# Kernel optimization log

Hardware: AMD Instinct MI355X
Metric: run time of the kernel (lower is better)

The kernel has to match this reference:

```python
import jax, jax.numpy as jnp
import numpy as np

H = 32          # total heads
K = 8           # active heads per token
D = 128         # head_dim = embed_dim // active_heads
E = 1024        # embed_dim
S = 1024        # seq_len
MAX_SEQ = 8192
BASE = 10000.0
SCALE = D ** -0.5
LB_W = 0.01
ENT_W = 0.01


def _rope(v, cos, sin):
    # v: (T, D); cos/sin: (T, D)
    v1, v2 = v[:, : D // 2], v[:, D // 2:]
    rot = jnp.concatenate([-v2, v1], axis=-1)
    return v * cos + rot * sin


def setup_inputs() -> dict:
    key = jax.random.key(0)
    ks = jax.random.split(key, 6)
    x = jax.random.normal(ks[0], (1, S, E), jnp.float32)
    Wq = jax.random.normal(ks[1], (E, H * D), jnp.float32) * 0.02
    Wk = jax.random.normal(ks[2], (E, H * D), jnp.float32) * 0.02
    Wv = jax.random.normal(ks[3], (E, H * D), jnp.float32) * 0.02
    Wr = jax.random.normal(ks[4], (E, H), jnp.float32) * 0.02
    Wo = jax.random.normal(ks[5], (K * D, E), jnp.float32) * 0.02
    head_counts = jnp.zeros((1, H), jnp.int32)
    return {"x": x, "Wq": Wq, "Wk": Wk, "Wv": Wv, "Wr": Wr, "Wo": Wo,
            "head_counts": head_counts}


def reference(x, Wq, Wk, Wv, Wr, Wo, head_counts):
    # ---- routing (eval mode: no gumbel noise) ----
    logits = x @ Wr                                   # (1, S, H)
    soft_probs = jax.nn.softmax(logits, axis=-1)
    top_logits, head_idx = jax.lax.top_k(logits, K)   # (1, S, K)
    head_w = jax.nn.softmax(top_logits, axis=-1)      # (1, S, K)

    # ---- aux loss ----
    primary = head_idx[..., 0]                        # (1, S)
    one_hot_p = jax.nn.one_hot(primary, H, dtype=jnp.float32)
    f = one_hot_p.mean(axis=1)                        # (1, H)
    p = soft_probs.mean(axis=1)                       # (1, H)
    balance = H * (f * p).sum(axis=-1).mean()
    entropy = -(soft_probs * jnp.log(soft_probs + 1e-8)).sum(axis=-1)
    entropy_loss = -entropy.mean()
    z_loss = (jax.nn.logsumexp(logits, axis=-1) ** 2).mean() * 0.01
    aux_loss = LB_W * balance + ENT_W * entropy_loss + z_loss

    # ---- projections + per-token gather of selected heads ----
    q_all = (x @ Wq).reshape(1, S, H, D)
    k_all = (x @ Wk).reshape(1, S, H, D)
    v_all = (x @ Wv).reshape(1, S, H, D)
    gidx = head_idx[..., None]                        # (1, S, K, 1)
    q = jnp.take_along_axis(q_all, gidx, axis=2)[0].reshape(S * K, D)
    k = jnp.take_along_axis(k_all, gidx, axis=2)[0].reshape(S * K, D)
    v = jnp.take_along_axis(v_all, gidx, axis=2)[0].reshape(S * K, D)

    heads_flat = head_idx[0].reshape(S * K)           # (T,)

    # rank of each dispatched token within its head (exclusive prefix count)
    oh = jax.nn.one_hot(heads_flat, H, dtype=jnp.int32)   # (T, H)
    excl = jnp.cumsum(oh, axis=0) - oh
    rank = jnp.take_along_axis(excl, heads_flat[:, None], axis=1)[:, 0]
    positions = rank + head_counts[0, heads_flat]
    positions = jnp.clip(positions, 0, MAX_SEQ - 1)

    # ---- per-head RoPE with per-head position counters ----
    inv_freq = 1.0 / (BASE ** (jnp.arange(0, D, 2, dtype=jnp.float32) / D))
    freqs = positions.astype(jnp.float32)[:, None] * inv_freq[None, :]
    emb = jnp.concatenate([freqs, freqs], axis=-1)    # (T, D)
    cos, sin = jnp.cos(emb), jnp.sin(emb)
    q = _rope(q, cos, sin)
    k = _rope(k, cos, sin)

    # ---- block-diagonal-causal attention (same head, earlier dispatch order) ----
    idx = jnp.arange(S * K)
    mask = (heads_flat[:, None] == heads_flat[None, :]) & (idx[None, :] <= idx[:, None])
    scores = (q @ k.T) * SCALE                        # (T, T)
    scores = jnp.where(mask, scores, jnp.float32(-1e30))
    attn = jax.nn.softmax(scores, axis=-1)
    out = attn @ v                                    # (T, D)

    # ---- combine with routing weights + output projection ----
    out = out.reshape(S, K, D) * head_w[0][..., None]
    out = out.reshape(S, K * D) @ Wo                  # (S, E)
    output = out[None]                                # (1, S, E)

    updated_counts = head_counts + oh.sum(axis=0)[None]
    return output, updated_counts, aux_loss
```

## Files before the change

kernel.cpp:

```cpp
#include <hip/hip_runtime.h>
#include <math.h>

#define S 1024
#define E 1024
#define H 32
#define KSEL 8
#define D 128
#define HD 4096
#define SK 8192
#define MAXL 1024
#define CAP 9216
#define ATTN_SCALE 0.08838834764831845f
#define SSTR 36
#define PSTR 40

typedef _Float16 half8 __attribute__((ext_vector_type(8)));
typedef _Float16 half4 __attribute__((ext_vector_type(4)));
typedef float floatx4 __attribute__((ext_vector_type(4)));
typedef float floatx16 __attribute__((ext_vector_type(16)));
typedef float f4 __attribute__((ext_vector_type(4)));

#define GLOAD_LDS16(gsrc, ldst) \
    __builtin_amdgcn_global_load_lds( \
        (const __attribute__((address_space(1))) void*)(gsrc), \
        (__attribute__((address_space(3))) void*)(ldst), 16, 0, 0)

__global__ __launch_bounds__(256) void router_kernel(
    const float* __restrict__ x, const float* __restrict__ Wr,
    int* __restrict__ head_idx, float* __restrict__ head_w,
    float* __restrict__ pbuf, float* __restrict__ entz,
    _Float16* __restrict__ xh)
{
    int tid = threadIdx.x;
    int s = blockIdx.x * 4 + (tid >> 6);
    int lane = tid & 63;
    int h = lane & 31, half = lane >> 5;
    const float* xr = x + (size_t)s * E + half * 512;
    const float* wr = Wr + (size_t)(half * 512) * H + h;
    float a0 = 0.f, a1 = 0.f, a2 = 0.f, a3 = 0.f;
    #pragma unroll 4
    for (int e = 0; e < 512; e += 4) {
        a0 += xr[e]     * wr[e * H];
        a1 += xr[e + 1] * wr[(e + 1) * H];
        a2 += xr[e + 2] * wr[(e + 2) * H];
        a3 += xr[e + 3] * wr[(e + 3) * H];
    }
    float acc = (a0 + a1) + (a2 + a3);
    acc += __shfl_xor(acc, 32, 64);
    float logit = acc;
    float m = logit;
    #pragma unroll
    for (int off = 16; off; off >>= 1) m = fmaxf(m, __shfl_xor(m, off, 64));
    float ex = expf(logit - m);
    float Z = ex;
    #pragma unroll
    for (int off = 16; off; off >>= 1) Z += __shfl_xor(Z, off, 64);
    float p = ex / Z;
    float es = p * logf(p + 1e-8f);
    #pragma unroll
    for (int off = 16; off; off >>= 1) es += __shfl_xor(es, off, 64);
    float lse = m + logf(Z);
    float lv = logit;
    float tv[KSEL]; int ti[KSEL];
    #pragma unroll
    for (int j = 0; j < KSEL; ++j) {
        float bv = lv; int bi = h;
        #pragma unroll
        for (int off = 16; off; off >>= 1) {
            float ov = __shfl_xor(bv, off, 64);
            int oi = __shfl_xor(bi, off, 64);
            if (ov > bv || (ov == bv && oi < bi)) { bv = ov; bi = oi; }
        }
        tv[j] = bv; ti[j] = bi;
        if (h == bi) lv = -INFINITY;
    }
    float Z2 = 0.f;
    #pragma unroll
    for (int j = 0; j < KSEL; ++j) Z2 += expf(tv[j] - tv[0]);
    if (lane < 32) pbuf[s * 32 + lane] = p;
    if (lane == 0) {
        entz[s * 2]     = es;
        entz[s * 2 + 1] = lse * lse;
        #pragma unroll
        for (int j = 0; j < KSEL; ++j) {
            head_idx[s * KSEL + j] = ti[j];
            head_w[s * KSEL + j]   = expf(tv[j] - tv[0]) / Z2;
        }
    }
    const float* xrow = x + (size_t)s * E;
    _Float16* xhrow = xh + (size_t)s * E;
    #pragma unroll
    for (int t = 0; t < 4; ++t) {
        int e = t * 256 + lane * 4;
        f4 v = *(const f4*)&xrow[e];
        half4 o;
        o.x = (_Float16)v.x; o.y = (_Float16)v.y; o.z = (_Float16)v.z; o.w = (_Float16)v.w;
        *(half4*)&xhrow[e] = o;
    }
}

__global__ __launch_bounds__(256) void order_conv_kernel(
    const int* __restrict__ head_idx, const int* __restrict__ head_counts,
    int* __restrict__ order, int* __restrict__ hlen, float* __restrict__ out_counts,
    const float* __restrict__ pbuf, const float* __restrict__ entz,
    float* __restrict__ out_aux,
    const float* __restrict__ Wq, const float* __restrict__ Wk,
    const float* __restrict__ Wv, const float* __restrict__ Wo,
    _Float16* __restrict__ Wqkt, _Float16* __restrict__ Wot)
{
    int bid = blockIdx.x, tid = threadIdx.x;
    if (bid >= 33) {
        int cb = bid - 33;
        int z = cb >> 10, rem = cb & 1023;
        if (z == 3 && (rem >> 4) >= 16) return;
        const float* W = (z == 0) ? Wq : (z == 1) ? Wk : (z == 2) ? Wv : Wo;
        _Float16* T = (z < 3) ? (Wqkt + (size_t)z * HD * E) : Wot;
        int C = (z < 3) ? HD : 1024;
        int r0 = (rem & 15) * 64, c0 = (rem >> 4) * 64;
        __shared__ float tile[64][65];
        #pragma unroll
        for (int p = 0; p < 4; ++p) {
            int idx = p * 256 + tid;
            int r = idx >> 4, cq = (idx & 15) * 4;
            f4 v = *(const f4*)&W[(size_t)(r0 + r) * C + c0 + cq];
            tile[r][cq] = v.x; tile[r][cq + 1] = v.y; tile[r][cq + 2] = v.z; tile[r][cq + 3] = v.w;
        }
        __syncthreads();
        #pragma unroll
        for (int p = 0; p < 2; ++p) {
            int idx = p * 256 + tid;
            int c = idx >> 3, r8 = (idx & 7) * 8;
            half8 o;
            #pragma unroll
            for (int j = 0; j < 8; ++j) o[j] = (_Float16)tile[r8 + j][c];
            *(half8*)&T[(size_t)(c0 + c) * 1024 + r0 + r8] = o;
        }
        return;
    }
    if (bid == H) {
        int hh = tid & 31, grp = tid >> 5;
        __shared__ float red[256], red2[256];
        __shared__ float psum[32];
        __shared__ int hist[32];
        if (tid < 32) hist[tid] = 0;
        float ps = 0.f;
        for (int s = grp; s < S; s += 8) ps += pbuf[s * 32 + hh];
        red[tid] = ps;
        float es = 0.f, zs = 0.f;
        for (int s = tid; s < S; s += 256) { es += entz[s * 2]; zs += entz[s * 2 + 1]; }
        red2[tid] = es;
        __syncthreads();
        if (grp == 0) {
            float v = 0.f;
            #pragma unroll
            for (int j = 0; j < 8; ++j) v += red[j * 32 + hh];
            psum[hh] = v;
        }
        __syncthreads();
        red[tid] = zs;
        for (int s = tid; s < S; s += 256)
            atomicAdd(&hist[head_idx[s * KSEL]], 1);
        __syncthreads();
        for (int stp = 128; stp; stp >>= 1) {
            if (tid < stp) { red[tid] += red[tid + stp]; red2[tid] += red2[tid + stp]; }
            __syncthreads();
        }
        if (tid == 0) {
            float bal = 0.f;
            for (int j = 0; j < H; ++j)
                bal += ((float)hist[j] / (float)S) * (psum[j] / (float)S);
            bal *= (float)H;
            float ent_loss = red2[0] / (float)S;
            float z = red[0] / (float)S * 0.01f;
            out_aux[0] = 0.01f * bal + 0.01f * ent_loss + z;
        }
        return;
    }
    int h = bid;
    int wave = tid >> 6, lane = tid & 63;
    __shared__ int wtot[4];
    int base = 0;
    int hc = head_counts[h];
    int v = head_idx[tid];
    for (int c0 = 0; c0 < SK; c0 += 256) {
        int vn = (c0 + 256 < SK) ? head_idx[c0 + 256 + tid] : 0;
        bool pred = (v == h);
        unsigned long long mask = __ballot(pred);
        int within = __popcll(mask & ((1ull << lane) - 1ull));
        if (lane == 0) wtot[wave] = __popcll(mask);
        __syncthreads();
        int pre = 0, tot = 0;
        #pragma unroll
        for (int w = 0; w < 4; ++w) { int t = wtot[w]; if (w < wave) pre += t; tot += t; }
        if (pred) order[h * MAXL + base + pre + within] = c0 + tid;
        base += tot;
        __syncthreads();
        v = vn;
    }
    if (tid == 0) {
        hlen[h] = base;
        out_counts[h] = (float)(hc + base);
    }
}

__global__ __launch_bounds__(256) void qkv_mfma(
    const _Float16* __restrict__ xh, const _Float16* __restrict__ Wt,
    const int* __restrict__ order, const int* __restrict__ hlen,
    const int* __restrict__ head_counts,
    _Float16* __restrict__ qh, _Float16* __restrict__ kh, _Float16* __restrict__ vT)
{
    int xid = blockIdx.x;
    int qkv = xid >> 5, h = xid & 31;
    int rt = blockIdx.y;
    int len = hlen[h];
    int row0 = rt * 64;
    if (row0 >= len) return;
    int hb = 0;
    for (int i = 0; i < h; ++i) hb += (hlen[i] + 31) & ~31;
    int lenp = (len + 31) & ~31;
    int tid = threadIdx.x, wave = tid >> 6, lane = tid & 63;
    int wm = wave >> 1, wn = wave & 1;
    int l32 = lane & 31, g = lane >> 5;

    __shared__ _Float16 Bs[2][128 * 64];

    int arow_g = row0 + wm * 32 + l32;
    int tok = (arow_g < len) ? (order[h * MAXL + arow_g] >> 3) : 0;
    const _Float16* aptr = xh + (size_t)tok * E;

    const _Float16* Wb = Wt + (size_t)((qkv * H + h) * D) * E;

    auto stageB = [&](int buf, int k0) {
        #pragma unroll
        for (int it = 0; it < 4; ++it) {
            int f = it * 256 + tid;
            int row = f >> 3, c = f & 7;
            int sc = c ^ (row & 7);
            const _Float16* src = Wb + (size_t)row * E + k0 + sc * 8;
            GLOAD_LDS16(src, &Bs[buf][f * 8]);
        }
    };

    floatx16 acc[2] = {};
    half8 a_cur[4], a_nxt[4];
    #pragma unroll
    for (int ks = 0; ks < 4; ++ks)
        a_cur[ks] = *(const half8*)(aptr + ks * 16 + g * 8);

    auto compute = [&](int buf, half8* a) {
        #pragma unroll
        for (int ks = 0; ks < 4; ++ks) {
            int wchunk = ks * 2 + g;
            #pragma unroll
            for (int nf = 0; nf < 2; ++nf) {
                int brow = wn * 64 + nf * 32 + l32;
                half8 bf = *(const half8*)&Bs[buf][brow * 64 + (wchunk ^ (brow & 7)) * 8];
                acc[nf] = __builtin_amdgcn_mfma_f32_32x32x16_f16(a[ks], bf, acc[nf], 0, 0, 0);
            }
        }
    };

    stageB(0, 0);
    __syncthreads();
    int buf = 0;
    for (int k0 = 64; k0 < E; k0 += 64) {
        stageB(buf ^ 1, k0);
        #pragma unroll
        for (int ks = 0; ks < 4; ++ks)
            a_nxt[ks] = *(const half8*)(aptr + k0 + ks * 16 + g * 8);
        compute(buf, a_cur);
        __syncthreads();
        buf ^= 1;
        #pragma unroll
        for (int ks = 0; ks < 4; ++ks) a_cur[ks] = a_nxt[ks];
    }
    compute(buf, a_cur);

    if (qkv < 2) {
        _Float16* dst = (qkv == 0) ? qh : kh;
        float* scr = (float*)&Bs[0][0];
        __syncthreads();
        #pragma unroll
        for (int nf = 0; nf < 2; ++nf) {
            int col = wn * 64 + nf * 32 + l32;
            #pragma unroll
            for (int reg = 0; reg < 16; ++reg) {
                int rl = wm * 32 + (reg & 3) + 8 * (reg >> 2) + 4 * g;
                scr[rl * 128 + col] = acc[nf][reg];
            }
        }
        __syncthreads();
        int hc = head_counts[h];
        #pragma unroll
        for (int pass = 0; pass < 16; ++pass) {
            int idx = pass * 256 + tid;
            int r = idx >> 6, d2 = idx & 63;
            int slot = row0 + r;
            if (slot < len) {
                float v1 = scr[r * 128 + d2], v2 = scr[r * 128 + 64 + d2];
                int p = slot + hc;
                p = p < 0 ? 0 : (p > 8191 ? 8191 : p);
                float inv = exp2f((float)d2 * -0.20762050f);
                float ang = (float)p * inv;
                float cs = cosf(ang), sn = sinf(ang);
                _Float16* dp = dst + ((size_t)hb + slot) * D;
                dp[d2]      = (_Float16)(v1 * cs - v2 * sn);
                dp[d2 + 64] = (_Float16)(v2 * cs + v1 * sn);
            }
        }
    } else {
        #pragma unroll
        for (int nf = 0; nf < 2; ++nf) {
            int col = wn * 64 + nf * 32 + l32;
            #pragma unroll
            for (int q4 = 0; q4 < 4; ++q4) {
                int slot0 = row0 + wm * 32 + 8 * q4 + 4 * g;
                _Float16* vp = vT + (size_t)hb * D + (size_t)col * lenp + slot0;
                if (slot0 + 3 < len) {
                    half4 o;
                    o.x = (_Float16)acc[nf][q4 * 4 + 0];
                    o.y = (_Float16)acc[nf][q4 * 4 + 1];
                    o.z = (_Float16)acc[nf][q4 * 4 + 2];
                    o.w = (_Float16)acc[nf][q4 * 4 + 3];
                    *(half4*)vp = o;
                } else {
                    #pragma unroll
                    for (int r2 = 0; r2 < 4; ++r2)
                        if (slot0 + r2 < len) vp[r2] = (_Float16)acc[nf][q4 * 4 + r2];
                }
            }
        }
    }
}

__global__ __launch_bounds__(128) void attn_mfma(
    const _Float16* __restrict__ qh, const _Float16* __restrict__ kh,
    const _Float16* __restrict__ vT,
    const int* __restrict__ order, const int* __restrict__ hlen,
    const float* __restrict__ head_w, _Float16* __restrict__ ao)
{
    int h = blockIdx.x >> 5, qt = blockIdx.x & 31;
    int len = hlen[h];
    int row0 = qt * 32;
    if (row0 >= len) return;
    int hb = 0;
    for (int i = 0; i < h; ++i) hb += (hlen[i] + 31) & ~31;
    int lenp = (len + 31) & ~31;
    int tid = threadIdx.x;
    int w = tid >> 6, lane = tid & 63;
    int l32 = lane & 31, g = lane >> 5;
    int srow = lane >> 1, shalf = lane & 1;

    __shared__ float Sld[2][32 * SSTR];
    __shared__ _Float16 Pld[2][32 * PSTR];
    __shared__ float alphaLd[2][32];
    __shared__ float mlLd[32][4];
    __shared__ float facLd[32][3];
    __shared__ int flatLd[32];
    __shared__ float Obuf[32][128];

    if (tid < 32) {
        int r = row0 + tid;
        flatLd[tid] = (r < len) ? order[h * MAXL + r] : -1;
    }

    const _Float16* qrow = qh + ((size_t)hb + row0 + l32) * D;
    half8 qf[8];
    #pragma unroll
    for (int t = 0; t < 8; ++t) qf[t] = *(const half8*)(qrow + t * 16 + g * 8);

    floatx16 O[4] = {};
    float m_run = -INFINITY, l_run = 0.f;

    if (w <= qt) {
        half8 kf[8], kfn[8], vv[8];
        {
            const _Float16* krow = kh + ((size_t)hb + w * 32 + l32) * D;
            #pragma unroll
            for (int t = 0; t < 8; ++t) kf[t] = *(const half8*)(krow + t * 16 + g * 8);
        }
        for (int kt = w; kt <= qt; kt += 2) {
            int col0 = kt * 32;
            floatx16 Sc = {};
            #pragma unroll
            for (int t = 0; t < 8; ++t)
                Sc = __builtin_amdgcn_mfma_f32_32x32x16_f16(qf[t], kf[t], Sc, 0, 0, 0);
            #pragma unroll
            for (int nt = 0; nt < 4; ++nt) {
                const _Float16* vp = vT + (size_t)hb * D + (size_t)(nt * 32 + l32) * lenp + col0;
                vv[nt * 2]     = *(const half8*)(vp + g * 8);
                vv[nt * 2 + 1] = *(const half8*)(vp + 16 + g * 8);
            }
            if (kt + 2 <= qt) {
                const _Float16* krow = kh + ((size_t)hb + col0 + 64 + l32) * D;
                #pragma unroll
                for (int t = 0; t < 8; ++t) kfn[t] = *(const half8*)(krow + t * 16 + g * 8);
            }
            bool diag = (kt == qt);
            #pragma unroll
            for (int reg = 0; reg < 16; ++reg) {
                int row = (reg & 3) + 8 * (reg >> 2) + 4 * g;
                float s = Sc[reg] * ATTN_SCALE;
                if (diag && l32 > row) s = -1e30f;
                Sld[w][row * SSTR + l32] = s;
            }
            __builtin_amdgcn_wave_barrier();
            const float* sp = &Sld[w][srow * SSTR + shalf * 16];
            float va[16];
            *(f4*)(va)      = *(const f4*)(sp);
            *(f4*)(va + 4)  = *(const f4*)(sp + 4);
            *(f4*)(va + 8)  = *(const f4*)(sp + 8);
            *(f4*)(va + 12) = *(const f4*)(sp + 12);
            float mt_ = va[0];
            #pragma unroll
            for (int j = 1; j < 16; ++j) mt_ = fmaxf(mt_, va[j]);
            mt_ = fmaxf(mt_, __shfl_xor(mt_, 1, 64));
            float m_new = fmaxf(m_run, mt_);
            float alpha = __expf(m_run - m_new);
            float p[16], tsum = 0.f;
            #pragma unroll
            for (int j = 0; j < 16; ++j) { p[j] = __expf(va[j] - m_new); tsum += p[j]; }
            tsum += __shfl_xor(tsum, 1, 64);
            l_run = l_run * alpha + tsum;
            m_run = m_new;
            half8 ph0, ph1;
            #pragma unroll
            for (int j = 0; j < 8; ++j) { ph0[j] = (_Float16)p[j]; ph1[j] = (_Float16)p[j + 8]; }
            *(half8*)&Pld[w][srow * PSTR + shalf * 16]     = ph0;
            *(half8*)&Pld[w][srow * PSTR + shalf * 16 + 8] = ph1;
            if (shalf == 0) alphaLd[w][srow] = alpha;
            __builtin_amdgcn_wave_barrier();
            f4 al[4];
            #pragma unroll
            for (int qq = 0; qq < 4; ++qq) al[qq] = *(const f4*)&alphaLd[w][4 * g + 8 * qq];
            #pragma unroll
            for (int reg = 0; reg < 16; ++reg) {
                float av = al[reg >> 2][reg & 3];
                O[0][reg] *= av; O[1][reg] *= av; O[2][reg] *= av; O[3][reg] *= av;
            }
            half8 pf0 = *(const half8*)&Pld[w][l32 * PSTR + g * 8];
            half8 pf1 = *(const half8*)&Pld[w][l32 * PSTR + 16 + g * 8];
            #pragma unroll
            for (int nt = 0; nt < 4; ++nt) {
                O[nt] = __builtin_amdgcn_mfma_f32_32x32x16_f16(pf0, vv[nt * 2],     O[nt], 0, 0, 0);
                O[nt] = __builtin_amdgcn_mfma_f32_32x32x16_f16(pf1, vv[nt * 2 + 1], O[nt], 0, 0, 0);
            }
            __builtin_amdgcn_wave_barrier();
            #pragma unroll
            for (int t = 0; t < 8; ++t) kf[t] = kfn[t];
        }
    }
    if (shalf == 0) { mlLd[srow][w * 2] = m_run; mlLd[srow][w * 2 + 1] = l_run; }
    __syncthreads();
    if (tid < 32) {
        float m0 = mlLd[tid][0], l0 = mlLd[tid][1];
        float m1 = mlLd[tid][2], l1 = mlLd[tid][3];
        float ms = fmaxf(m0, m1);
        float f0 = __expf(m0 - ms), f1 = __expf(m1 - ms);
        float lt = f0 * l0 + f1 * l1;
        int flat = flatLd[tid];
        float hw = (flat >= 0) ? head_w[flat] : 0.f;
        facLd[tid][0] = f1;
        facLd[tid][1] = hw / lt;
        facLd[tid][2] = f0;
    }
    __syncthreads();
    if (w == 1) {
        #pragma unroll
        for (int nt = 0; nt < 4; ++nt) {
            int col = nt * 32 + l32;
            #pragma unroll
            for (int reg = 0; reg < 16; ++reg) {
                int row = (reg & 3) + 8 * (reg >> 2) + 4 * g;
                Obuf[row][col] = O[nt][reg] * facLd[row][0];
            }
        }
    }
    __syncthreads();
    if (w == 0) {
        #pragma unroll
        for (int nt = 0; nt < 4; ++nt) {
            int col = nt * 32 + l32;
            #pragma unroll
            for (int reg = 0; reg < 16; ++reg) {
                int row = (reg & 3) + 8 * (reg >> 2) + 4 * g;
                int flat = flatLd[row];
                if (flat >= 0) {
                    float val = (O[nt][reg] * facLd[row][2] + Obuf[row][col]) * facLd[row][1];
                    ao[(size_t)flat * D + col] = (_Float16)val;
                }
            }
        }
    }
}

__global__ __launch_bounds__(256) void out_mfma(
    const _Float16* __restrict__ A, const _Float16* __restrict__ Bt,
    float* __restrict__ C)
{
    int n0 = blockIdx.x * 64, m0 = blockIdx.y * 64;
    int tid = threadIdx.x, wave = tid >> 6, lane = tid & 63;
    int wm = wave >> 1, wn = wave & 1;
    int l32 = lane & 31, g = lane >> 5;

    __shared__ _Float16 Bs[2][64 * 64];

    const _Float16* aptr = A + (size_t)(m0 + wm * 32 + l32) * 1024;

    auto stageB = [&](int buf, int k0) {
        #pragma unroll
        for (int it = 0; it < 2; ++it) {
            int f = it * 256 + tid;
            int row = f >> 3, c = f & 7;
            int sc = c ^ (row & 7);
            GLOAD_LDS16(Bt + (size_t)(n0 + row) * 1024 + k0 + sc * 8, &Bs[buf][f * 8]);
        }
    };

    floatx16 acc = {};
    int brow = wn * 32 + l32;
    half8 a_cur[4], a_nxt[4];
    #pragma unroll
    for (int ks = 0; ks < 4; ++ks)
        a_cur[ks] = *(const half8*)(aptr + ks * 16 + g * 8);

    auto compute = [&](int buf, half8* a) {
        #pragma unroll
        for (int ks = 0; ks < 4; ++ks) {
            int wchunk = ks * 2 + g;
            half8 bf = *(const half8*)&Bs[buf][brow * 64 + (wchunk ^ (brow & 7)) * 8];
            acc = __builtin_amdgcn_mfma_f32_32x32x16_f16(a[ks], bf, acc, 0, 0, 0);
        }
    };

    stageB(0, 0);
    __syncthreads();
    int buf = 0;
    for (int k0 = 64; k0 < 1024; k0 += 64) {
        stageB(buf ^ 1, k0);
        #pragma unroll
        for (int ks = 0; ks < 4; ++ks)
            a_nxt[ks] = *(const half8*)(aptr + k0 + ks * 16 + g * 8);
        compute(buf, a_cur);
        __syncthreads();
        buf ^= 1;
        #pragma unroll
        for (int ks = 0; ks < 4; ++ks) a_cur[ks] = a_nxt[ks];
    }
    compute(buf, a_cur);

    int col = n0 + wn * 32 + l32;
    #pragma unroll
    for (int reg = 0; reg < 16; ++reg) {
        int row = m0 + wm * 32 + (reg & 3) + 8 * (reg >> 2) + 4 * g;
        C[(size_t)row * 1024 + col] = acc[reg];
    }
}

extern "C" void kernel_launch(void* const* d_in, const int* in_sizes, int n_in,
                              void* d_out, int out_size, void* d_ws, size_t ws_size,
                              hipStream_t stream)
{
    const float* x  = (const float*)d_in[0];
    const float* Wq = (const float*)d_in[1];
    const float* Wk = (const float*)d_in[2];
    const float* Wv = (const float*)d_in[3];
    const float* Wr = (const float*)d_in[4];
    const float* Wo = (const float*)d_in[5];
    const int* head_counts = (const int*)d_in[6];
    float* out = (float*)d_out;

    float* head_w = (float*)d_ws;
    float* pbuf   = head_w + SK;
    float* entz   = pbuf + S * 32;
    int* head_idx = (int*)(entz + S * 2);
    int* order    = head_idx + SK;
    int* hlen     = order + H * MAXL;
    _Float16* xh   = (_Float16*)(hlen + 64);
    _Float16* aoh  = xh + (size_t)S * E;
    _Float16* Wqkt = aoh + (size_t)SK * D;
    _Float16* Wot  = Wqkt + (size_t)3 * HD * E;
    _Float16* qh   = Wot + (size_t)1024 * 1024;
    _Float16* kh   = qh + (size_t)CAP * D;
    _Float16* vT   = kh + (size_t)CAP * D;

    router_kernel<<<S / 4, 256, 0, stream>>>(x, Wr, head_idx, head_w, pbuf, entz, xh);
    order_conv_kernel<<<33 + 4096, 256, 0, stream>>>(head_idx, head_counts, order, hlen,
                                                     out + (size_t)S * E, pbuf, entz,
                                                     out + (size_t)S * E + H,
                                                     Wq, Wk, Wv, Wo, Wqkt, Wot);
    qkv_mfma<<<dim3(96, 16), 256, 0, stream>>>(xh, Wqkt, order, hlen, head_counts,
                                               qh, kh, vT);
    attn_mfma<<<H * 32, 128, 0, stream>>>(qh, kh, vT, order, hlen, head_w, aoh);
    out_mfma<<<dim3(16, 16), 256, 0, stream>>>(aoh, Wot, out);
}
```

Measured before the change: 220.1 us.

## Move weight conversion into router kernel and batch per-head scan chunks

The fp32-to-fp16 weight transpose/convert work moves out of the order kernel and into the router kernel as extra blocks. It now uses 128x128 fp16 tiles with an XOR-swizzled LDS layout instead of 64x64 fp32 tiles, so conversion overlaps routing and the scan kernel no longer waits behind 4000+ conversion blocks. The per-head order scan handles four 256-element chunks per iteration, cutting the number of barrier round trips by four. The risk is larger LDS use per conversion block (32KB) and fewer, heavier blocks.

```diff
diff --git a/kernel.cpp b/kernel.cpp
--- a/kernel.cpp
+++ b/kernel.cpp
@@ -14,6 +14,9 @@
 #define SSTR 36
 #define PSTR 40
 
+#define NROUTER 256
+#define NCONV 832
+
 typedef _Float16 half8 __attribute__((ext_vector_type(8)));
 typedef _Float16 half4 __attribute__((ext_vector_type(4)));
 typedef float floatx4 __attribute__((ext_vector_type(4)));
@@ -25,14 +28,54 @@
         (const __attribute__((address_space(1))) void*)(gsrc), \
         (__attribute__((address_space(3))) void*)(ldst), 16, 0, 0)
 
-__global__ __launch_bounds__(256) void router_kernel(
+__global__ __launch_bounds__(256) void router_conv_kernel(
     const float* __restrict__ x, const float* __restrict__ Wr,
     int* __restrict__ head_idx, float* __restrict__ head_w,
     float* __restrict__ pbuf, float* __restrict__ entz,
-    _Float16* __restrict__ xh)
+    _Float16* __restrict__ xh,
+    const float* __restrict__ Wq, const float* __restrict__ Wk,
+    const float* __restrict__ Wv, const float* __restrict__ Wo,
+    _Float16* __restrict__ Wqkt, _Float16* __restrict__ Wot)
 {
-    int tid = threadIdx.x;
-    int s = blockIdx.x * 4 + (tid >> 6);
+    int bid = blockIdx.x, tid = threadIdx.x;
+    if (bid >= NROUTER) {
+        __shared__ _Float16 tl[128 * 128];
+        int cb = bid - NROUTER;
+        int z, rem;
+        if (cb < 768) { z = cb >> 8; rem = cb & 255; }
+        else          { z = 3;       rem = cb - 768; }
+        const float* W = (z == 0) ? Wq : (z == 1) ? Wk : (z == 2) ? Wv : Wo;
+        _Float16* T = (z < 3) ? (Wqkt + (size_t)z * HD * E) : Wot;
+        int C = (z < 3) ? HD : 1024;
+        int nc = C >> 7;
+        int c0 = (rem % nc) * 128;
+        int r0 = (rem / nc) * 128;
+        #pragma unroll
+        for (int p = 0; p < 16; ++p) {
+            int idx = p * 256 + tid;
+            int rr = idx >> 5, cg = (idx & 31) * 4;
+            f4 v = *(const f4*)&W[(size_t)(r0 + rr) * C + c0 + cg];
+            half4 o;
+            o.x = (_Float16)v.x; o.y = (_Float16)v.y;
+            o.z = (_Float16)v.z; o.w = (_Float16)v.w;
+            int sc = cg ^ (((rr >> 3) & 7) << 2);
+            *(half4*)&tl[rr * 128 + sc] = o;
+        }
+        __syncthreads();
+        #pragma unroll
+        for (int p = 0; p < 8; ++p) {
+            int chunk = p * 256 + tid;
+            int cc = chunk >> 4, ch = chunk & 15;
+            int cidx = cc ^ ((ch & 7) << 2);
+            half8 o;
+            #pragma unroll
+            for (int j = 0; j < 8; ++j)
+                o[j] = tl[(ch * 8 + j) * 128 + cidx];
+            *(half8*)&T[(size_t)(c0 + cc) * 1024 + r0 + ch * 8] = o;
+        }
+        return;
+    }
+    int s = bid * 4 + (tid >> 6);
     int lane = tid & 63;
     int h = lane & 31, half = lane >> 5;
     const float* xr = x + (size_t)s * E + half * 512;
@@ -99,44 +142,13 @@
     }
 }
 
-__global__ __launch_bounds__(256) void order_conv_kernel(
+__global__ __launch_bounds__(256) void scan_aux_kernel(
     const int* __restrict__ head_idx, const int* __restrict__ head_counts,
     int* __restrict__ order, int* __restrict__ hlen, float* __restrict__ out_counts,
     const float* __restrict__ pbuf, const float* __restrict__ entz,
-    float* __restrict__ out_aux,
-    const float* __restrict__ Wq, const float* __restrict__ Wk,
-    const float* __restrict__ Wv, const float* __restrict__ Wo,
-    _Float16* __restrict__ Wqkt, _Float16* __restrict__ Wot)
+    float* __restrict__ out_aux)
 {
     int bid = blockIdx.x, tid = threadIdx.x;
-    if (bid >= 33) {
-        int cb = bid - 33;
-        int z = cb >> 10, rem = cb & 1023;
-        if (z == 3 && (rem >> 4) >= 16) return;
-        const float* W = (z == 0) ? Wq : (z == 1) ? Wk : (z == 2) ? Wv : Wo;
-        _Float16* T = (z < 3) ? (Wqkt + (size_t)z * HD * E) : Wot;
-        int C = (z < 3) ? HD : 1024;
-        int r0 = (rem & 15) * 64, c0 = (rem >> 4) * 64;
-        __shared__ float tile[64][65];
-        #pragma unroll
-        for (int p = 0; p < 4; ++p) {
-            int idx = p * 256 + tid;
-            int r = idx >> 4, cq = (idx & 15) * 4;
-            f4 v = *(const f4*)&W[(size_t)(r0 + r) * C + c0 + cq];
-            tile[r][cq] = v.x; tile[r][cq + 1] = v.y; tile[r][cq + 2] = v.z; tile[r][cq + 3] = v.w;
-        }
-        __syncthreads();
-        #pragma unroll
-        for (int p = 0; p < 2; ++p) {
-            int idx = p * 256 + tid;
-            int c = idx >> 3, r8 = (idx & 7) * 8;
-            half8 o;
-            #pragma unroll
-            for (int j = 0; j < 8; ++j) o[j] = (_Float16)tile[r8 + j][c];
-            *(half8*)&T[(size_t)(c0 + c) * 1024 + r0 + r8] = o;
-        }
-        return;
-    }
     if (bid == H) {
         int hh = tid & 31, grp = tid >> 5;
         __shared__ float red[256], red2[256];
@@ -178,24 +190,47 @@
     }
     int h = bid;
     int wave = tid >> 6, lane = tid & 63;
-    __shared__ int wtot[4];
+    __shared__ int wtot[4][4];
     int base = 0;
     int hc = head_counts[h];
-    int v = head_idx[tid];
-    for (int c0 = 0; c0 < SK; c0 += 256) {
-        int vn = (c0 + 256 < SK) ? head_idx[c0 + 256 + tid] : 0;
-        bool pred = (v == h);
-        unsigned long long mask = __ballot(pred);
-        int within = __popcll(mask & ((1ull << lane) - 1ull));
-        if (lane == 0) wtot[wave] = __popcll(mask);
-        __syncthreads();
-        int pre = 0, tot = 0;
-        #pragma unroll
-        for (int w = 0; w < 4; ++w) { int t = wtot[w]; if (w < wave) pre += t; tot += t; }
-        if (pred) order[h * MAXL + base + pre + within] = c0 + tid;
-        base += tot;
-        __syncthreads();
-        v = vn;
+    int v0 = head_idx[tid],       v1 = head_idx[256 + tid];
+    int v2 = head_idx[512 + tid], v3 = head_idx[768 + tid];
+    unsigned long long lt = (1ull << lane) - 1ull;
+    for (int c0 = 0; c0 < SK; c0 += 1024) {
+        int n0 = 0, n1 = 0, n2 = 0, n3 = 0;
+        if (c0 + 1024 < SK) {
+            n0 = head_idx[c0 + 1024 + tid]; n1 = head_idx[c0 + 1280 + tid];
+            n2 = head_idx[c0 + 1536 + tid]; n3 = head_idx[c0 + 1792 + tid];
+        }
+        bool p0 = (v0 == h), p1 = (v1 == h), p2 = (v2 == h), p3 = (v3 == h);
+        unsigned long long m0 = __ballot(p0), m1 = __ballot(p1);
+        unsigned long long m2 = __ballot(p2), m3 = __ballot(p3);
+        int w0 = __popcll(m0 & lt), w1 = __popcll(m1 & lt);
+        int w2 = __popcll(m2 & lt), w3 = __popcll(m3 & lt);
+        if (lane == 0) {
+            wtot[0][wave] = __popcll(m0); wtot[1][wave] = __popcll(m1);
+            wtot[2][wave] = __popcll(m2); wtot[3][wave] = __popcll(m3);
+        }
+        __syncthreads();
+        int pw[4], T[4];
+        #pragma unroll
+        for (int i = 0; i < 4; ++i) {
+            int pre = 0, tot = 0;
+            #pragma unroll
+            for (int w = 0; w < 4; ++w) {
+                int tv = wtot[i][w];
+                if (w < wave) pre += tv;
+                tot += tv;
+            }
+            pw[i] = pre; T[i] = tot;
+        }
+        if (p0) order[h * MAXL + base + pw[0] + w0] = c0 + tid;
+        if (p1) order[h * MAXL + base + T[0] + pw[1] + w1] = c0 + 256 + tid;
+        if (p2) order[h * MAXL + base + T[0] + T[1] + pw[2] + w2] = c0 + 512 + tid;
+        if (p3) order[h * MAXL + base + T[0] + T[1] + T[2] + pw[3] + w3] = c0 + 768 + tid;
+        base += T[0] + T[1] + T[2] + T[3];
+        __syncthreads();
+        v0 = n0; v1 = n1; v2 = n2; v3 = n3;
     }
     if (tid == 0) {
         hlen[h] = base;
@@ -584,11 +619,11 @@
     _Float16* kh   = qh + (size_t)CAP * D;
     _Float16* vT   = kh + (size_t)CAP * D;
 
-    router_kernel<<<S / 4, 256, 0, stream>>>(x, Wr, head_idx, head_w, pbuf, entz, xh);
-    order_conv_kernel<<<33 + 4096, 256, 0, stream>>>(head_idx, head_counts, order, hlen,
-                                                     out + (size_t)S * E, pbuf, entz,
-                                                     out + (size_t)S * E + H,
-                                                     Wq, Wk, Wv, Wo, Wqkt, Wot);
+    router_conv_kernel<<<NROUTER + NCONV, 256, 0, stream>>>(
+        x, Wr, head_idx, head_w, pbuf, entz, xh, Wq, Wk, Wv, Wo, Wqkt, Wot);
+    scan_aux_kernel<<<33, 256, 0, stream>>>(head_idx, head_counts, order, hlen,
+                                            out + (size_t)S * E, pbuf, entz,
+                                            out + (size_t)S * E + H);
     qkv_mfma<<<dim3(96, 16), 256, 0, stream>>>(xh, Wqkt, order, hlen, head_counts,
                                                qh, kh, vT);
     attn_mfma<<<H * 32, 128, 0, stream>>>(qh, kh, vT, order, hlen, head_w, aoh);
```

Result: no change. 222.4 us (+1.1%).
